# Optimization experiments

Measured on AMD Instinct MI355X. Metric: run time of the kernel, lower is better.

Reference implementation:

```python
import jax, jax.numpy as jnp
import numpy as np


def _assignment(rows, n_clusters, portion, dtype):
    # eye(n_clusters) repeat_interleaved `portion` times along rows, truncated to `rows`,
    # plus the same matrix rolled down by `portion` rows (overlapping assignment).
    s = (jnp.arange(rows)[:, None] // portion == jnp.arange(n_clusters)[None, :]).astype(dtype)
    return s + jnp.roll(s, portion, axis=0)


def _dense_gcn(x, adj, W, b):
    # PyG DenseGCNConv: set diag to 1 (self loops), symmetric deg^-1/2 normalization,
    # out = A_norm @ (x W) + b
    n = adj.shape[0]
    idx = jnp.arange(n)
    adj = adj.at[idx, idx].set(1.0)
    out = x @ W
    d = jnp.clip(jnp.sum(adj, axis=-1), 1.0, None) ** -0.5
    adj = d[:, None] * adj * d[None, :]
    return adj @ out + b


def setup_inputs() -> dict:
    key = jax.random.key(0)
    ks = jax.random.split(key, 8)
    N, D, H, O = 4096, 128, 128, 2
    x = jax.random.normal(ks[0], (N, D), dtype=jnp.float32)
    edge_index = jax.random.uniform(ks[1], (2, N, N), dtype=jnp.float32)  # [1] slice = dense adjacency
    ca1 = jax.random.normal(ks[2], (D, D), dtype=jnp.float32) * (1.414 / np.sqrt(D))  # xavier_normal gain 1.414
    W1 = jax.random.normal(ks[3], (D, H), dtype=jnp.float32) * 0.05
    b1 = jnp.zeros((H,), dtype=jnp.float32)
    W2 = jax.random.normal(ks[4], (H, H), dtype=jnp.float32) * 0.05
    b2 = jnp.zeros((H,), dtype=jnp.float32)
    Wlin = jax.random.normal(ks[5], (O, H), dtype=jnp.float32) * 0.05
    blin = jnp.zeros((O,), dtype=jnp.float32)
    return {"x": x, "edge_index": edge_index, "num_nodes1": 2048,
            "ca1": ca1, "W1": W1, "b1": b1, "W2": W2, "b2": b2,
            "Wlin": Wlin, "blin": blin}


def reference(x, edge_index, num_nodes1, ca1, W1, b1, W2, b2, Wlin, blin):
    N = x.shape[0]
    nearest = N + (N % 2)
    n1 = nearest // 2
    n2 = n1
    portion1 = -(-nearest // n1)  # ceil
    dt = x.dtype

    # level-1 overlapping assignment [N, n1]
    flat_s = _assignment(N, n1, portion1, dt)
    newadj = edge_index[1]
    x1 = flat_s.T @ x                       # [n1, D]
    adj1 = flat_s.T @ newadj @ flat_s       # [n1, n1]

    # cross-layer masked attention
    reverse_s = 1.0 - flat_s
    scores = (x1 @ ca1) @ x.T * reverse_s.T  # [n1, N]
    alpha = jax.nn.softmax(scores, axis=1)
    x1 = alpha @ x + x1

    # GCN layer 1 (dropout is identity in eval mode)
    h = jax.nn.relu(_dense_gcn(x1, adj1, W1, b1))  # [n1, H]

    # level-2 pooling
    portion2 = -(-nearest // n2)
    flat_s2 = _assignment(h.shape[0], n2, portion2, dt)  # [n1, n2]
    x2 = flat_s2.T @ h
    adj2 = flat_s2.T @ adj1 @ flat_s2

    h2 = _dense_gcn(x2, adj2, W2, b2)  # [n2, H]
    out = jnp.mean(h2, axis=0, keepdims=True)  # mean over nodes -> [1, H]
    out = jax.nn.relu(out @ Wlin.T + blin)     # [1, O]
    return jax.nn.log_softmax(out, axis=1)
```

## Files before the change

kernel.cpp:

```cpp
#include <hip/hip_runtime.h>

typedef float  f32x4 __attribute__((ext_vector_type(4)));
typedef float  f32x2 __attribute__((ext_vector_type(2)));
typedef short  short8v __attribute__((ext_vector_type(8)));

static __device__ __forceinline__ unsigned short f2bf(float f) {
  union { float f; unsigned u; } v; v.f = f;
  unsigned r = v.u + 0x7FFFu + ((v.u >> 16) & 1u);
  return (unsigned short)(r >> 16);
}
static __device__ __forceinline__ float bf2f(unsigned short h) {
  union { unsigned u; float f; } v; v.u = ((unsigned)h) << 16;
  return v.f;
}
static __device__ __forceinline__ f32x4 mfma16(short8v a, short8v b, f32x4 c) {
  return __builtin_amdgcn_mfma_f32_16x16x32_bf16(a, b, c, 0, 0, 0);
}

static __device__ __forceinline__ size_t pidx(int r, int c, int C) {
  return (((size_t)(r >> 4) * (C >> 5) + (c >> 5)) << 9) +
         ((size_t)((((c >> 3) & 3) << 4) + (r & 15)) << 3) + (c & 7);
}

static __device__ __forceinline__ float elt(const float* r, int c) { return r[c]; }
static __device__ __forceinline__ float elt(const unsigned short* r, int c) { return bf2f(r[c]); }

template <int NF>
static __device__ __forceinline__ void load_f(const float* row, int c0, float* f) {
  #pragma unroll
  for (int u = 0; u < (NF - 2) / 4; ++u)
    *(f32x4*)(f + 4 * u) = *(const f32x4*)(row + c0 + 4 * u);
  *(f32x2*)(f + NF - 2) = *(const f32x2*)(row + c0 + NF - 2);
}
template <int NF>
static __device__ __forceinline__ void load_f(const unsigned short* row, int c0, float* f) {
  #pragma unroll
  for (int u = 0; u < NF / 2; ++u) {
    unsigned a = *(const unsigned*)(row + c0 + 2 * u);
    f[2 * u]     = bf2f((unsigned short)a);
    f[2 * u + 1] = bf2f((unsigned short)(a >> 16));
  }
}

template <typename T, int KCNT>
static __device__ void pool_adj_body(const T* __restrict__ in,
                                     unsigned short* __restrict__ outh,
                                     unsigned short* __restrict__ outp,
                                     float* __restrict__ rs,
                                     float* __restrict__ diag,
                                     int n, int nin, int bid, float* red) {
  constexpr int NF = 2 * KCNT + 2;
  int chunk = n >> 3;
  int j = (bid & 7) * chunk + (bid >> 3);
  int r0 = 2 * j;
  const T* row0 = in + (size_t)((r0 + 0) & (nin - 1)) * nin;
  const T* row1 = in + (size_t)((r0 + 1) & (nin - 1)) * nin;
  const T* row2 = in + (size_t)((r0 + 2) & (nin - 1)) * nin;
  const T* row3 = in + (size_t)((r0 + 3) & (nin - 1)) * nin;
  int t = threadIdx.x;
  int k0 = t * KCNT;
  int c0 = 2 * k0;
  float F[NF];
  if (c0 + NF <= nin) {
    float f[NF];
    load_f<NF>(row0, c0, F);
    load_f<NF>(row1, c0, f);
    #pragma unroll
    for (int u = 0; u < NF; ++u) F[u] += f[u];
    load_f<NF>(row2, c0, f);
    #pragma unroll
    for (int u = 0; u < NF; ++u) F[u] += f[u];
    load_f<NF>(row3, c0, f);
    #pragma unroll
    for (int u = 0; u < NF; ++u) F[u] += f[u];
  } else {
    #pragma unroll
    for (int u = 0; u < NF; ++u) {
      int c = (c0 + u) & (nin - 1);
      F[u] = elt(row0, c) + elt(row1, c) + elt(row2, c) + elt(row3, c);
    }
  }
  float pr[KCNT + 1];
  #pragma unroll
  for (int m = 0; m <= KCNT; ++m) pr[m] = F[2 * m] + F[2 * m + 1];
  float racc = 0.f;
  unsigned short hv[KCNT];
  #pragma unroll
  for (int kl = 0; kl < KCNT; ++kl) {
    float s = pr[kl] + pr[kl + 1];
    hv[kl] = f2bf(s);
    racc += s;
    if (k0 + kl == j) diag[j] = s;
  }
  if constexpr (KCNT == 8) {
    short8v o8;
    #pragma unroll
    for (int kl = 0; kl < 8; ++kl) o8[kl] = (short)hv[kl];
    if (outh) *(short8v*)&outh[(size_t)j * n + k0] = o8;
    *(short8v*)&outp[pidx(j, k0, n)] = o8;
  } else {
    uint2 o4;
    o4.x = (unsigned)hv[0] | ((unsigned)hv[1] << 16);
    o4.y = (unsigned)hv[2] | ((unsigned)hv[3] << 16);
    if (outh) *(uint2*)&outh[(size_t)j * n + k0] = o4;
    *(uint2*)&outp[pidx(j, k0, n)] = o4;
  }
  #pragma unroll
  for (int o = 32; o > 0; o >>= 1) racc += __shfl_xor(racc, o);
  if ((threadIdx.x & 63) == 0) red[threadIdx.x >> 6] = racc;
  __syncthreads();
  if (threadIdx.x == 0) rs[j] = red[0] + red[1] + red[2] + red[3];
}

static __device__ void split_body(const float* __restrict__ X,
                                  unsigned short* __restrict__ Kph,
                                  unsigned short* __restrict__ Kpl,
                                  unsigned short* __restrict__ Vp,
                                  int bb) {
  #pragma unroll
  for (int r = 0; r < 4; ++r) {
    int e = bb * 1024 + r * 256 + threadIdx.x;
    int i = e >> 7, d = e & 127;
    float v = X[e];
    unsigned short hi = f2bf(v);
    Kph[pidx(i, d, 128)] = hi;
    Kpl[pidx(i, d, 128)] = f2bf(v - bf2f(hi));
    Vp[pidx(d, i, 4096)] = hi;
  }
}

static __device__ __forceinline__ void gemm16x128(const float (*xs)[128],
                                                  const float* __restrict__ W,
                                                  int d, float* acc) {
  #pragma unroll
  for (int i = 0; i < 16; ++i) acc[i] = 0.f;
  for (int e = 0; e < 128; e += 4) {
    float w0 = W[(e + 0) * 128 + d];
    float w1 = W[(e + 1) * 128 + d];
    float w2 = W[(e + 2) * 128 + d];
    float w3 = W[(e + 3) * 128 + d];
    #pragma unroll
    for (int i = 0; i < 16; ++i) {
      f32x4 xv = *(const f32x4*)&xs[i][e];
      float a = acc[i];
      a = fmaf(xv[0], w0, a);
      a = fmaf(xv[1], w1, a);
      a = fmaf(xv[2], w2, a);
      a = fmaf(xv[3], w3, a);
      acc[i] = a;
    }
  }
}

static __device__ __forceinline__ void gemm8x128(const float (*xs)[128], int ibase,
                                                 const float* __restrict__ W,
                                                 int d, float* acc) {
  #pragma unroll
  for (int i = 0; i < 8; ++i) acc[i] = 0.f;
  for (int e = 0; e < 128; e += 4) {
    float w0 = W[(e + 0) * 128 + d];
    float w1 = W[(e + 1) * 128 + d];
    float w2 = W[(e + 2) * 128 + d];
    float w3 = W[(e + 3) * 128 + d];
    #pragma unroll
    for (int i = 0; i < 8; ++i) {
      f32x4 xv = *(const f32x4*)&xs[ibase + i][e];
      float a = acc[i];
      a = fmaf(xv[0], w0, a);
      a = fmaf(xv[1], w1, a);
      a = fmaf(xv[2], w2, a);
      a = fmaf(xv[3], w3, a);
      acc[i] = a;
    }
  }
}

static __device__ void gemm_q_body(const float* __restrict__ x,
                                   const float* __restrict__ W,
                                   float* __restrict__ x1b,
                                   unsigned short* __restrict__ Qph,
                                   unsigned short* __restrict__ Qpl,
                                   int tile, float (*xs)[128], int d) {
  int r0 = tile * 16;
  #pragma unroll
  for (int i = 0; i < 16; ++i) {
    int rr = 2 * (r0 + i);
    float v = x[(size_t)((rr + 0) & 4095) * 128 + d] + x[(size_t)((rr + 1) & 4095) * 128 + d] +
              x[(size_t)((rr + 2) & 4095) * 128 + d] + x[(size_t)((rr + 3) & 4095) * 128 + d];
    xs[i][d] = v;
    x1b[(size_t)(r0 + i) * 128 + d] = v;
  }
  __syncthreads();
  float acc[16];
  gemm16x128(xs, W, d, acc);
  #pragma unroll
  for (int i = 0; i < 16; ++i) {
    size_t o = pidx(r0 + i, d, 128);
    unsigned short hi = f2bf(acc[i]);
    Qph[o] = hi;
    Qpl[o] = f2bf(acc[i] - bf2f(hi));
  }
}

__global__ __launch_bounds__(256) void prep_kernel(const float* __restrict__ x,
                                                   unsigned short* __restrict__ Kph,
                                                   unsigned short* __restrict__ Kpl,
                                                   unsigned short* __restrict__ Vp,
                                                   const float* __restrict__ ca1,
                                                   float* __restrict__ x1b,
                                                   unsigned short* __restrict__ Qph,
                                                   unsigned short* __restrict__ Qpl) {
  __shared__ __align__(16) char smem[16384];
  int b = blockIdx.x;
  if (b < 512) {
    split_body(x, Kph, Kpl, Vp, b);
  } else {
    int half = threadIdx.x >> 7, d = threadIdx.x & 127;
    float (*xs)[128] = (float (*)[128])(smem + half * 8192);
    gemm_q_body(x, ca1, x1b, Qph, Qpl, (b - 512) * 2 + half, xs, d);
  }
}

static __device__ void flash_body(const short8v* __restrict__ Qh8,
                                  const short8v* __restrict__ Ql8,
                                  const short8v* __restrict__ Kh8,
                                  const short8v* __restrict__ Kl8,
                                  const short8v* __restrict__ V8,
                                  uint2* __restrict__ pacc2,
                                  float* __restrict__ pm,
                                  float* __restrict__ pl,
                                  int jt, int kc, int lane,
                                  unsigned short (*P)[32]) {
  int q = lane & 15, g = lane >> 4;
  int j = jt * 16 + q;
  int kbase = kc * 256;
  int twoj = 2 * j;

  short8v qh[4], ql[4];
  #pragma unroll
  for (int c = 0; c < 4; ++c) {
    qh[c] = Qh8[(size_t)(jt * 4 + c) * 64 + lane];
    ql[c] = Ql8[(size_t)(jt * 4 + c) * 64 + lane];
  }
  float m = -1e30f, l = 0.f;
  f32x4 acc[8];
  #pragma unroll
  for (int t = 0; t < 8; ++t) acc[t] = (f32x4){0.f, 0.f, 0.f, 0.f};

  for (int step = 0; step < 8; ++step) {
    int kt = kbase + step * 32;
    size_t fa = (size_t)(kt >> 4) * 4;
    f32x4 z = {0.f, 0.f, 0.f, 0.f};
    f32x4 hh0 = z, hl0 = z, lh0 = z, hh1 = z, hl1 = z, lh1 = z;
    __builtin_amdgcn_s_setprio(1);
    #pragma unroll
    for (int c = 0; c < 4; ++c) {
      short8v ah = Kh8[(fa + c) * 64 + lane];
      short8v al = Kl8[(fa + c) * 64 + lane];
      short8v bh = Kh8[(fa + 4 + c) * 64 + lane];
      short8v bl = Kl8[(fa + 4 + c) * 64 + lane];
      hh0 = mfma16(ah, qh[c], hh0);
      hh1 = mfma16(bh, qh[c], hh1);
      hl0 = mfma16(ah, ql[c], hl0);
      hl1 = mfma16(bh, ql[c], hl1);
      lh0 = mfma16(al, qh[c], lh0);
      lh1 = mfma16(bl, qh[c], lh1);
    }
    __builtin_amdgcn_s_setprio(0);
    short8v vfrag[8];
    #pragma unroll
    for (int t = 0; t < 8; ++t)
      vfrag[t] = V8[((size_t)t * 128 + (kt >> 5)) * 64 + lane];

    f32x4 s0 = hh0 + hl0 + lh0;
    f32x4 s1 = hh1 + hl1 + lh1;
    float sv[8];
    #pragma unroll
    for (int r = 0; r < 4; ++r) {
      int k0 = kt + g * 4 + r;
      float v0 = s0[r];
      if (((k0 - twoj) & 4095) < 4) v0 = 0.f;
      sv[r] = v0;
      int k1 = k0 + 16;
      float v1 = s1[r];
      if (((k1 - twoj) & 4095) < 4) v1 = 0.f;
      sv[4 + r] = v1;
    }
    float cmx = sv[0];
    #pragma unroll
    for (int r = 1; r < 8; ++r) cmx = fmaxf(cmx, sv[r]);
    cmx = fmaxf(cmx, __shfl_xor(cmx, 16));
    cmx = fmaxf(cmx, __shfl_xor(cmx, 32));
    float mnew = fmaxf(m, cmx);
    float ps = 0.f;
    unsigned short pb[8];
    #pragma unroll
    for (int r = 0; r < 8; ++r) {
      float pv = __expf(sv[r] - mnew);
      ps += pv;
      pb[r] = f2bf(pv);
    }
    ps += __shfl_xor(ps, 16);
    ps += __shfl_xor(ps, 32);
    if (__any(cmx > m)) {
      float scl = __expf(m - mnew);
      l *= scl;
      float sc0 = __shfl(scl, 4 * g + 0);
      float sc1 = __shfl(scl, 4 * g + 1);
      float sc2 = __shfl(scl, 4 * g + 2);
      float sc3 = __shfl(scl, 4 * g + 3);
      #pragma unroll
      for (int t = 0; t < 8; ++t) {
        acc[t][0] *= sc0; acc[t][1] *= sc1; acc[t][2] *= sc2; acc[t][3] *= sc3;
      }
    }
    m = mnew;
    l += ps;
    *(unsigned*)&P[q][4 * g]          = (unsigned)pb[0] | ((unsigned)pb[1] << 16);
    *(unsigned*)&P[q][4 * g + 2]      = (unsigned)pb[2] | ((unsigned)pb[3] << 16);
    *(unsigned*)&P[q][16 + 4 * g]     = (unsigned)pb[4] | ((unsigned)pb[5] << 16);
    *(unsigned*)&P[q][16 + 4 * g + 2] = (unsigned)pb[6] | ((unsigned)pb[7] << 16);
    __syncthreads();
    short8v pa = *(const short8v*)&P[q][8 * g];
    __builtin_amdgcn_s_setprio(1);
    #pragma unroll
    for (int t = 0; t < 8; ++t) acc[t] = mfma16(pa, vfrag[t], acc[t]);
    __builtin_amdgcn_s_setprio(0);
    __syncthreads();
  }
  size_t tau = (size_t)jt * 16 + kc;
  #pragma unroll
  for (int t = 0; t < 8; ++t) {
    uint2 o;
    o.x = (unsigned)f2bf(acc[t][0]) | ((unsigned)f2bf(acc[t][1]) << 16);
    o.y = (unsigned)f2bf(acc[t][2]) | ((unsigned)f2bf(acc[t][3]) << 16);
    pacc2[(tau * 8 + t) * 64 + lane] = o;
  }
  if (g == 0) {
    pm[(size_t)j * 16 + kc] = m;
    pl[(size_t)j * 16 + kc] = l;
  }
}

__global__ __launch_bounds__(256) void megaB_kernel(const float* __restrict__ newadj,
                                                    unsigned short* __restrict__ adj1h,
                                                    unsigned short* __restrict__ adj1p,
                                                    float* __restrict__ rs1,
                                                    float* __restrict__ diag1,
                                                    const short8v* __restrict__ Qh8,
                                                    const short8v* __restrict__ Ql8,
                                                    const short8v* __restrict__ Kh8,
                                                    const short8v* __restrict__ Kl8,
                                                    const short8v* __restrict__ V8,
                                                    uint2* __restrict__ pacc2,
                                                    float* __restrict__ pm,
                                                    float* __restrict__ pl) {
  __shared__ __align__(16) char smem[4096];
  int b = blockIdx.x;
  if (b < 512) {
    int w = threadIdx.x >> 6, lane = threadIdx.x & 63;
    int kc = b & 15;
    int jt = (b >> 4) * 4 + w;
    unsigned short (*P)[32] = (unsigned short (*)[32])(smem + w * 1024);
    flash_body(Qh8, Ql8, Kh8, Kl8, V8, pacc2, pm, pl, jt, kc, lane, P);
  } else {
    pool_adj_body<float, 8>(newadj, adj1h, adj1p, rs1, diag1, 2048, 4096, b - 512, (float*)smem);
  }
}

__global__ __launch_bounds__(256) void combine_gemm_kernel(const uint4* __restrict__ pacc4,
                                                           const float* __restrict__ pm,
                                                           const float* __restrict__ pl,
                                                           const float* __restrict__ x1b,
                                                           const float* __restrict__ W,
                                                           const float* __restrict__ rs,
                                                           const float* __restrict__ diag,
                                                           float* __restrict__ yB,
                                                           unsigned short* __restrict__ ypack,
                                                           int M) {
  __shared__ unsigned short pL[32768];
  __shared__ float pmL[256], plL[256];
  __shared__ float xs[16][128];
  int jt = blockIdx.x;
  int r0 = jt * 16;
  int tid = threadIdx.x;
  const uint4* src = pacc4 + (size_t)jt * 4096;
  uint4* dst = (uint4*)pL;
  #pragma unroll
  for (int u = 0; u < 16; ++u) dst[u * 256 + tid] = src[u * 256 + tid];
  pmL[tid] = pm[(size_t)r0 * 16 + tid];
  plL[tid] = pl[(size_t)r0 * 16 + tid];
  __syncthreads();
  int h = tid >> 7, d = tid & 127;
  int t = d >> 4, q = d & 15;
  #pragma unroll
  for (int ii = 0; ii < 8; ++ii) {
    int i = h * 8 + ii;
    int j = r0 + i;
    int g = i >> 2, r = i & 3;
    int off = t * 256 + (g * 16 + q) * 4 + r;
    float Mx = -1e30f;
    #pragma unroll
    for (int c = 0; c < 16; ++c) Mx = fmaxf(Mx, pmL[i * 16 + c]);
    float L = 0.f, o = 0.f;
    #pragma unroll
    for (int c = 0; c < 16; ++c) {
      float w = __expf(pmL[i * 16 + c] - Mx);
      L += plL[i * 16 + c] * w;
      o += w * bf2f(pL[c * 2048 + off]);
    }
    xs[i][d] = o / L + x1b[(size_t)j * 128 + d];
  }
  __syncthreads();
  float acc[8];
  gemm8x128(xs, h * 8, W, d, acc);
  short8v t0;
  #pragma unroll
  for (int ii = 0; ii < 8; ++ii) {
    int j = r0 + h * 8 + ii;
    float dv = rsqrtf(fmaxf(rs[j] - diag[j] + 1.f, 1.f));
    float v = acc[ii] * dv;
    yB[(size_t)j * 128 + d] = v;
    t0[ii] = (short)f2bf(v);
  }
  *(short8v*)&ypack[pidx(d, r0 + h * 8, M)] = t0;
}

static __device__ void mfma_tile_body(const short8v* __restrict__ A8,
                                      const short8v* __restrict__ B8,
                                      float* __restrict__ C, int K32, int M,
                                      int jt, int nt, int ks, int lane) {
  int q = lane & 15, g = lane >> 4;
  int half = K32 >> 1;
  const short8v* ap = A8 + ((size_t)jt * K32 + ks * half) * 64 + lane;
  const short8v* bp = B8 + ((size_t)nt * K32 + ks * half) * 64 + lane;
  f32x4 acc = {0.f, 0.f, 0.f, 0.f};
  for (int kc = 0; kc < half; kc += 4) {
    #pragma unroll
    for (int u = 0; u < 4; ++u)
      acc = mfma16(ap[(size_t)(kc + u) * 64], bp[(size_t)(kc + u) * 64], acc);
  }
  float* Cp = C + (size_t)ks * M * 128;
  #pragma unroll
  for (int r = 0; r < 4; ++r)
    Cp[(size_t)(jt * 16 + g * 4 + r) * 128 + nt * 16 + q] = acc[r];
}

__global__ __launch_bounds__(256) void mega2_kernel(const unsigned short* __restrict__ adj1h,
                                                    const short8v* __restrict__ adj1p8,
                                                    const short8v* __restrict__ yp8,
                                                    float* __restrict__ G,
                                                    unsigned short* __restrict__ adj2p,
                                                    float* __restrict__ rs2,
                                                    float* __restrict__ diag2,
                                                    unsigned* __restrict__ cnt) {
  __shared__ float red[4];
  int b = blockIdx.x;
  if (b == 0 && threadIdx.x == 0) *cnt = 0;
  if (b < 512) {
    int fid = b * 4 + (threadIdx.x >> 6);
    int jt = fid & 127, nt = (fid >> 7) & 7, ks = fid >> 10;
    mfma_tile_body(adj1p8, yp8, G, 64, 2048, jt, nt, ks, threadIdx.x & 63);
  } else {
    pool_adj_body<unsigned short, 4>(adj1h, nullptr, adj2p, rs2, diag2, 1024, 2048, b - 512, red);
  }
}

static __device__ __forceinline__ float epi_h(const float* __restrict__ G,
                                              const float* __restrict__ y,
                                              const float* __restrict__ rs,
                                              const float* __restrict__ diag,
                                              const float* __restrict__ bias,
                                              int n, int r, int d, bool relu) {
  float dv = rsqrtf(fmaxf(rs[r] - diag[r] + 1.f, 1.f));
  float gs = G[(size_t)r * 128 + d] + G[(size_t)(n + r) * 128 + d];
  float v = dv * (gs + (1.f - diag[r]) * y[(size_t)r * 128 + d]) + bias[d];
  return relu ? fmaxf(v, 0.f) : v;
}

__global__ __launch_bounds__(128) void epi_final_kernel(const float* __restrict__ G,
                                                        const float* __restrict__ yB,
                                                        const float* __restrict__ rs1,
                                                        const float* __restrict__ diag1,
                                                        const float* __restrict__ b1,
                                                        const float* __restrict__ W,
                                                        const float* __restrict__ rs2,
                                                        const float* __restrict__ diag2,
                                                        const float* __restrict__ b2,
                                                        const unsigned short* __restrict__ adj2p,
                                                        float* __restrict__ part,
                                                        unsigned* __restrict__ cnt,
                                                        const float* __restrict__ Wlin,
                                                        const float* __restrict__ blin,
                                                        float* __restrict__ out,
                                                        int n1) {
  __shared__ float xs[8][128];
  __shared__ float wred[16][8];
  __shared__ float uval[8];
  __shared__ float rr0[128], rr1[128];
  __shared__ unsigned doneS;
  int b = blockIdx.x;
  int tid = threadIdx.x;
  int r0 = b * 8;
  {
    const unsigned short* base = adj2p + (size_t)(b >> 2) * 512 + (size_t)(b & 3) * 128 + tid;
    int s = tid >> 3;
    float wacc = 0.f;
    for (int mm = 0; mm < 64; ++mm) {
      int r = mm * 16 + s;
      float d2r = rsqrtf(fmaxf(rs2[r] - diag2[r] + 1.f, 1.f));
      wacc += d2r * bf2f(base[(size_t)mm * 16384]);
    }
    wred[s][tid & 7] = wacc;
  }
  __syncthreads();
  if (tid < 8) {
    float wsum = 0.f;
    #pragma unroll
    for (int s2 = 0; s2 < 16; ++s2) wsum += wred[s2][tid];
    int k = r0 + tid;
    float d2k = rsqrtf(fmaxf(rs2[k] - diag2[k] + 1.f, 1.f));
    uval[tid] = wsum + d2k * (1.f - diag2[k]);
  }
  int d = tid;
  #pragma unroll
  for (int i = 0; i < 8; ++i) {
    int rr = 2 * (r0 + i);
    float s = 0.f;
    #pragma unroll
    for (int a = 0; a < 4; ++a)
      s += epi_h(G, yB, rs1, diag1, b1, n1, (rr + a) & (n1 - 1), d, true);
    xs[i][d] = s;
  }
  __syncthreads();
  float acc[8];
  gemm8x128(xs, 0, W, d, acc);
  float pd = 0.f;
  #pragma unroll
  for (int i = 0; i < 8; ++i) {
    int j = r0 + i;
    float dv = rsqrtf(fmaxf(rs2[j] - diag2[j] + 1.f, 1.f));
    pd += uval[i] * (acc[i] * dv);
  }
  part[(size_t)b * 128 + d] = pd;
  __threadfence();
  __syncthreads();
  if (tid == 0) doneS = atomicAdd(cnt, 1u);
  __syncthreads();
  if (doneS == 127) {
    __threadfence();
    float cs = 0.f;
    for (int bb = 0; bb < 128; ++bb) cs += part[(size_t)bb * 128 + d];
    float mean = cs * (1.f / 2048.f) + b2[d];
    rr0[d] = mean * Wlin[d];
    rr1[d] = mean * Wlin[128 + d];
    __syncthreads();
    for (int sred = 64; sred > 0; sred >>= 1) {
      if (tid < sred) { rr0[tid] += rr0[tid + sred]; rr1[tid] += rr1[tid + sred]; }
      __syncthreads();
    }
    if (tid == 0) {
      float z0 = fmaxf(rr0[0] + blin[0], 0.f);
      float z1 = fmaxf(rr1[0] + blin[1], 0.f);
      float mz = fmaxf(z0, z1);
      float lse = mz + logf(__expf(z0 - mz) + __expf(z1 - mz));
      out[0] = z0 - lse;
      out[1] = z1 - lse;
    }
  }
}

extern "C" void kernel_launch(void* const* d_in, const int* in_sizes, int n_in,
                              void* d_out, int out_size, void* d_ws, size_t ws_size,
                              hipStream_t stream) {
  const float* x      = (const float*)d_in[0];
  const float* eidx   = (const float*)d_in[1];
  const float* newadj = eidx + (size_t)4096 * 4096;
  const float* ca1    = (const float*)d_in[3];
  const float* W1     = (const float*)d_in[4];
  const float* b1     = (const float*)d_in[5];
  const float* W2     = (const float*)d_in[6];
  const float* b2     = (const float*)d_in[7];
  const float* Wlin   = (const float*)d_in[8];
  const float* blin   = (const float*)d_in[9];
  float* out = (float*)d_out;

  if (ws_size < 42u * 1024u * 1024u) return;

  char* p = (char*)d_ws;
  auto alloc = [&](size_t bytes) -> char* {
    char* r = p; p += (bytes + 255) & ~(size_t)255; return r;
  };
  unsigned short* adj1h = (unsigned short*)alloc((size_t)2048 * 2048 * 2);
  unsigned short* adj1p = (unsigned short*)alloc((size_t)2048 * 2048 * 2);
  float* d1raw = (float*)alloc(2048 * 4);
  float* diag1 = (float*)alloc(2048 * 4);
  float* x1b   = (float*)alloc((size_t)2048 * 128 * 4);
  unsigned short* Qph = (unsigned short*)alloc((size_t)2048 * 128 * 2);
  unsigned short* Qpl = (unsigned short*)alloc((size_t)2048 * 128 * 2);
  unsigned short* Kph = (unsigned short*)alloc((size_t)4096 * 128 * 2);
  unsigned short* Kpl = (unsigned short*)alloc((size_t)4096 * 128 * 2);
  unsigned short* Vp  = (unsigned short*)alloc((size_t)4096 * 128 * 2);
  float* pmB   = (float*)alloc((size_t)2048 * 16 * 4);
  float* plB   = (float*)alloc((size_t)2048 * 16 * 4);
  uint2* pacc2 = (uint2*)alloc((size_t)2048 * 8 * 64 * 8);
  float* yB    = (float*)alloc((size_t)2048 * 128 * 4);
  unsigned short* ypack = (unsigned short*)alloc((size_t)2048 * 128 * 2);
  float* G     = (float*)alloc((size_t)2 * 2048 * 128 * 4);
  unsigned short* adj2p = (unsigned short*)alloc((size_t)1024 * 1024 * 2);
  float* d2raw = (float*)alloc(1024 * 4);
  float* diag2 = (float*)alloc(1024 * 4);
  float* part  = (float*)alloc((size_t)128 * 128 * 4);
  unsigned* cnt = (unsigned*)alloc(256);

  prep_kernel<<<576, 256, 0, stream>>>(x, Kph, Kpl, Vp, ca1, x1b, Qph, Qpl);
  megaB_kernel<<<2560, 256, 0, stream>>>(newadj, adj1h, adj1p, d1raw, diag1,
                                         (const short8v*)Qph, (const short8v*)Qpl,
                                         (const short8v*)Kph, (const short8v*)Kpl,
                                         (const short8v*)Vp, pacc2, pmB, plB);
  combine_gemm_kernel<<<128, 256, 0, stream>>>((const uint4*)pacc2, pmB, plB,
                                               x1b, W1, d1raw, diag1, yB, ypack, 2048);
  mega2_kernel<<<1536, 256, 0, stream>>>(adj1h, (const short8v*)adj1p, (const short8v*)ypack,
                                         G, adj2p, d2raw, diag2, cnt);
  epi_final_kernel<<<128, 128, 0, stream>>>(G, yB, d1raw, diag1, b1, W2,
                                            d2raw, diag2, b2, adj2p,
                                            part, cnt, Wlin, blin, out, 2048);
}
```

Before: 108.5 us.

## Move adjacency pooling into prep kernel and run flash attention standalone

```diff
diff --git a/kernel.cpp b/kernel.cpp
--- a/kernel.cpp
+++ b/kernel.cpp
@@ -202,35 +202,45 @@
   }
 }
 
-__global__ __launch_bounds__(256) void prep_kernel(const float* __restrict__ x,
-                                                   unsigned short* __restrict__ Kph,
-                                                   unsigned short* __restrict__ Kpl,
-                                                   unsigned short* __restrict__ Vp,
-                                                   const float* __restrict__ ca1,
-                                                   float* __restrict__ x1b,
-                                                   unsigned short* __restrict__ Qph,
-                                                   unsigned short* __restrict__ Qpl) {
+__global__ __launch_bounds__(256) void mega1_kernel(const float* __restrict__ newadj,
+                                                    unsigned short* __restrict__ adj1h,
+                                                    unsigned short* __restrict__ adj1p,
+                                                    float* __restrict__ rs1,
+                                                    float* __restrict__ diag1,
+                                                    const float* __restrict__ x,
+                                                    unsigned short* __restrict__ Kph,
+                                                    unsigned short* __restrict__ Kpl,
+                                                    unsigned short* __restrict__ Vp,
+                                                    const float* __restrict__ ca1,
+                                                    float* __restrict__ x1b,
+                                                    unsigned short* __restrict__ Qph,
+                                                    unsigned short* __restrict__ Qpl) {
   __shared__ __align__(16) char smem[16384];
   int b = blockIdx.x;
   if (b < 512) {
     split_body(x, Kph, Kpl, Vp, b);
-  } else {
+  } else if (b < 576) {
     int half = threadIdx.x >> 7, d = threadIdx.x & 127;
     float (*xs)[128] = (float (*)[128])(smem + half * 8192);
     gemm_q_body(x, ca1, x1b, Qph, Qpl, (b - 512) * 2 + half, xs, d);
-  }
-}
-
-static __device__ void flash_body(const short8v* __restrict__ Qh8,
-                                  const short8v* __restrict__ Ql8,
-                                  const short8v* __restrict__ Kh8,
-                                  const short8v* __restrict__ Kl8,
-                                  const short8v* __restrict__ V8,
-                                  uint2* __restrict__ pacc2,
-                                  float* __restrict__ pm,
-                                  float* __restrict__ pl,
-                                  int jt, int kc, int lane,
-                                  unsigned short (*P)[32]) {
+  } else {
+    pool_adj_body<float, 8>(newadj, adj1h, adj1p, rs1, diag1, 2048, 4096, b - 576, (float*)smem);
+  }
+}
+
+__global__ __launch_bounds__(256) void flash_kernel(const short8v* __restrict__ Qh8,
+                                                    const short8v* __restrict__ Ql8,
+                                                    const short8v* __restrict__ Kh8,
+                                                    const short8v* __restrict__ Kl8,
+                                                    const short8v* __restrict__ V8,
+                                                    uint2* __restrict__ pacc2,
+                                                    float* __restrict__ pm,
+                                                    float* __restrict__ pl) {
+  __shared__ unsigned short Pbuf[4][16][32];
+  int w = threadIdx.x >> 6, lane = threadIdx.x & 63;
+  int kc = blockIdx.x & 15;
+  int jt = (blockIdx.x >> 4) * 4 + w;
+  unsigned short (*P)[32] = Pbuf[w];
   int q = lane & 15, g = lane >> 4;
   int j = jt * 16 + q;
   int kbase = kc * 256;
@@ -339,32 +349,6 @@
   if (g == 0) {
     pm[(size_t)j * 16 + kc] = m;
     pl[(size_t)j * 16 + kc] = l;
-  }
-}
-
-__global__ __launch_bounds__(256) void megaB_kernel(const float* __restrict__ newadj,
-                                                    unsigned short* __restrict__ adj1h,
-                                                    unsigned short* __restrict__ adj1p,
-                                                    float* __restrict__ rs1,
-                                                    float* __restrict__ diag1,
-                                                    const short8v* __restrict__ Qh8,
-                                                    const short8v* __restrict__ Ql8,
-                                                    const short8v* __restrict__ Kh8,
-                                                    const short8v* __restrict__ Kl8,
-                                                    const short8v* __restrict__ V8,
-                                                    uint2* __restrict__ pacc2,
-                                                    float* __restrict__ pm,
-                                                    float* __restrict__ pl) {
-  __shared__ __align__(16) char smem[4096];
-  int b = blockIdx.x;
-  if (b < 512) {
-    int w = threadIdx.x >> 6, lane = threadIdx.x & 63;
-    int kc = b & 15;
-    int jt = (b >> 4) * 4 + w;
-    unsigned short (*P)[32] = (unsigned short (*)[32])(smem + w * 1024);
-    flash_body(Qh8, Ql8, Kh8, Kl8, V8, pacc2, pm, pl, jt, kc, lane, P);
-  } else {
-    pool_adj_body<float, 8>(newadj, adj1h, adj1p, rs1, diag1, 2048, 4096, b - 512, (float*)smem);
   }
 }
 
@@ -613,11 +597,11 @@
   float* part  = (float*)alloc((size_t)128 * 128 * 4);
   unsigned* cnt = (unsigned*)alloc(256);
 
-  prep_kernel<<<576, 256, 0, stream>>>(x, Kph, Kpl, Vp, ca1, x1b, Qph, Qpl);
-  megaB_kernel<<<2560, 256, 0, stream>>>(newadj, adj1h, adj1p, d1raw, diag1,
-                                         (const short8v*)Qph, (const short8v*)Qpl,
-                                         (const short8v*)Kph, (const short8v*)Kpl,
-                                         (const short8v*)Vp, pacc2, pmB, plB);
+  mega1_kernel<<<2624, 256, 0, stream>>>(newadj, adj1h, adj1p, d1raw, diag1,
+                                         x, Kph, Kpl, Vp, ca1, x1b, Qph, Qpl);
+  flash_kernel<<<512, 256, 0, stream>>>((const short8v*)Qph, (const short8v*)Qpl,
+                                        (const short8v*)Kph, (const short8v*)Kpl,
+                                        (const short8v*)Vp, pacc2, pmB, plB);
   combine_gemm_kernel<<<128, 256, 0, stream>>>((const uint4*)pacc2, pmB, plB,
                                                x1b, W1, d1raw, diag1, yB, ypack, 2048);
   mega2_kernel<<<1536, 256, 0, stream>>>(adj1h, (const short8v*)adj1p, (const short8v*)ypack,
```

New measurement: 99.46 us (median of 2 runs). 1.09x faster.
